# Performance work log

Measured on AMD Instinct MI355X. Metric: run time of the kernel, lower is better.

## Reference

```python
import jax, jax.numpy as jnp
import numpy as np
import math

B, T, D, H, FF, L, CS, LC = 8, 512, 512, 8, 2048, 6, 16, 4
DK = D // H
MIN16 = float(np.finfo(np.float16).min)  # masked_fill value used by the module


def _chunk_mask(size, ck, n_left):
    # subsequent_chunk_mask: row i attends [max((i//ck - n_left)*ck, 0), (i//ck + 1)*ck)
    i = np.arange(size)
    j = np.arange(size)
    ci = i // ck
    start = np.maximum((ci - n_left) * ck, 0)
    end = (ci + 1) * ck
    return (j[None, :] >= start[:, None]) & (j[None, :] < end[:, None])


def setup_inputs() -> dict:
    key = jax.random.key(0)
    ks = jax.random.split(key, 16)
    s = 0.02
    rn = lambda k, shp: jax.random.normal(k, shp, jnp.float32) * s
    xs = jax.random.normal(ks[0], (B, T, D), jnp.float32)
    # RelPositionalEncoding sinusoidal table
    pos = np.arange(T, dtype=np.float32)[:, None]
    div = np.exp(np.arange(0, D, 2, dtype=np.float32) * (-math.log(10000.0) / D))
    pe = np.zeros((T, D), np.float32)
    pe[:, 0::2] = np.sin(pos * div)
    pe[:, 1::2] = np.cos(pos * div)
    pos_emb = jnp.asarray(pe)[None]  # (1, T, D)
    mask = jnp.asarray(_chunk_mask(T, CS, LC))[None]  # (1, T, T) bool, True=attend
    return {
        'xs': xs, 'pos_emb': pos_emb, 'mask': mask,
        'Wq': rn(ks[1], (L, D, D)), 'bq': jnp.zeros((L, D)),
        'Wk': rn(ks[2], (L, D, D)), 'bk': jnp.zeros((L, D)),
        'Wv': rn(ks[3], (L, D, D)), 'bv': jnp.zeros((L, D)),
        'Wo': rn(ks[4], (L, D, D)), 'bo': jnp.zeros((L, D)),
        'Wp': rn(ks[5], (L, D, D)),
        'pbu': rn(ks[6], (L, H, DK)), 'pbv': rn(ks[7], (L, H, DK)),
        'ln1_s': jnp.ones((L, D)), 'ln1_b': jnp.zeros((L, D)),
        'ln2_s': jnp.ones((L, D)), 'ln2_b': jnp.zeros((L, D)),
        'W1': rn(ks[8], (L, D, FF)), 'b1': jnp.zeros((L, FF)),
        'W2': rn(ks[9], (L, FF, D)), 'b2': jnp.zeros((L, D)),
        'lnf_s': jnp.ones((D,)), 'lnf_b': jnp.zeros((D,)),
    }


def _ln(x, g, b):
    m = jnp.mean(x, -1, keepdims=True)
    v = jnp.var(x, -1, keepdims=True)
    return (x - m) * jax.lax.rsqrt(v + 1e-5) * g + b


def reference(xs, pos_emb, mask, Wq, bq, Wk, bk, Wv, bv, Wo, bo, Wp, pbu, pbv,
              ln1_s, ln1_b, ln2_s, ln2_b, W1, b1, W2, b2, lnf_s, lnf_b):
    x = xs * math.sqrt(D)          # xscale from positional encoding
    m = mask[:, None, :, :]        # (1,1,T,T)
    scale = 1.0 / math.sqrt(DK)
    for l in range(L):
        h = _ln(x, ln1_s[l], ln1_b[l])
        q = (h @ Wq[l] + bq[l]).reshape(B, T, H, DK)                       # (B,T,H,DK)
        k = (h @ Wk[l] + bk[l]).reshape(B, T, H, DK).transpose(0, 2, 1, 3)  # (B,H,T,DK)
        v = (h @ Wv[l] + bv[l]).reshape(B, T, H, DK).transpose(0, 2, 1, 3)
        p = (pos_emb @ Wp[l]).reshape(T, H, DK).transpose(1, 0, 2)          # (H,T,DK)
        qu = (q + pbu[l]).transpose(0, 2, 1, 3)  # (B,H,T,DK)
        qv = (q + pbv[l]).transpose(0, 2, 1, 3)
        ac = jnp.einsum('bhtd,bhsd->bhts', qu, k)
        bd = jnp.einsum('bhtd,hsd->bhts', qv, p)
        scores = jnp.where(m, (ac + bd) * scale, MIN16)
        attn = jnp.where(m, jax.nn.softmax(scores, axis=-1), 0.0)
        o = jnp.einsum('bhts,bhsd->bthd', attn, v).reshape(B, T, D)
        x = x + o @ Wo[l] + bo[l]
        h2 = _ln(x, ln2_s[l], ln2_b[l])
        x = x + jax.nn.relu(h2 @ W1[l] + b1[l]) @ W2[l] + b2[l]
    return _ln(x, lnf_s, lnf_b)
```

## Files before the change

### kernel.cpp

```cpp
#include <hip/hip_runtime.h>

#define B_ 8
#define T_ 512
#define D_ 512
#define H_ 8
#define FF_ 2048
#define L_ 6
#define CS_ 16
#define LC_ 4
#define DK_ 64
#define MT_ (B_*T_)

typedef unsigned short u16;
typedef __attribute__((ext_vector_type(8))) short bf8_t;
typedef __attribute__((ext_vector_type(4))) float f4_t;

__device__ __forceinline__ float bf2f(u16 u){
  union { unsigned int i; float f; } c; c.i = ((unsigned int)u) << 16; return c.f;
}
__device__ __forceinline__ u16 f2bf(float f){
  union { float f; unsigned int i; } c; c.f = f;
  unsigned int x = c.i;
  return (u16)((x + 0x7FFFu + ((x >> 16) & 1u)) >> 16);
}

__global__ void init_kernel(const float* __restrict__ xs, const float* __restrict__ pe,
                            float* __restrict__ x, u16* __restrict__ pe_bf)
{
  int stride = gridDim.x * blockDim.x;
  int i0 = blockIdx.x * blockDim.x + threadIdx.x;
  const float s = 22.62741699796952f;
  for (int i = i0; i < B_*T_*D_; i += stride) x[i] = xs[i] * s;
  for (int i = i0; i < T_*D_;    i += stride) pe_bf[i] = f2bf(pe[i]);
}

__global__ void transpose_kernel(const float* __restrict__ in, u16* __restrict__ out,
                                 int K, int N)
{
  __shared__ float tile[32][33];
  int l = blockIdx.z;
  const float* src = in + (size_t)l * K * N;
  u16* dst = out + (size_t)l * N * K;
  int n0 = blockIdx.x * 32, k0 = blockIdx.y * 32;
  int tx = threadIdx.x, ty = threadIdx.y;
  #pragma unroll
  for (int i = 0; i < 4; ++i)
    tile[ty + i*8][tx] = src[(size_t)(k0 + ty + i*8) * N + n0 + tx];
  __syncthreads();
  #pragma unroll
  for (int i = 0; i < 4; ++i)
    dst[(size_t)(n0 + ty + i*8) * K + k0 + tx] = f2bf(tile[tx][ty + i*8]);
}

__global__ void transpose_qkv_kernel(const float* __restrict__ Wq, const float* __restrict__ Wk,
                                     const float* __restrict__ Wv, u16* __restrict__ out)
{
  __shared__ float tile[32][33];
  int l = blockIdx.z;
  int n0 = blockIdx.x * 32, k0 = blockIdx.y * 32;
  const float* W = (n0 < 512) ? Wq : (n0 < 1024 ? Wk : Wv);
  int nn0 = n0 & 511;
  const float* src = W + (size_t)l * D_ * D_;
  u16* dst = out + (size_t)l * 3 * D_ * D_;
  int tx = threadIdx.x, ty = threadIdx.y;
  #pragma unroll
  for (int i = 0; i < 4; ++i)
    tile[ty + i*8][tx] = src[(size_t)(k0 + ty + i*8) * D_ + nn0 + tx];
  __syncthreads();
  #pragma unroll
  for (int i = 0; i < 4; ++i)
    dst[(size_t)(n0 + ty + i*8) * D_ + k0 + tx] = f2bf(tile[tx][ty + i*8]);
}

__global__ void pack_bias_kernel(const float* __restrict__ bq, const float* __restrict__ bk,
                                 const float* __restrict__ bv, float* __restrict__ out)
{
  int l = blockIdx.x, t = threadIdx.x;
  out[l*1536 + t]        = bq[l*512 + t];
  out[l*1536 + 512  + t] = bk[l*512 + t];
  out[l*1536 + 1024 + t] = bv[l*512 + t];
}

template <int OUTMODE>
__global__ __launch_bounds__(256) void ln_kernel(const float* __restrict__ x,
    const float* __restrict__ g, const float* __restrict__ b, void* __restrict__ outp)
{
  int row = blockIdx.x;
  const float* xr = x + (size_t)row * D_;
  int t = threadIdx.x;
  float v0 = xr[t], v1 = xr[t + 256];
  float s = v0 + v1, s2 = v0*v0 + v1*v1;
  #pragma unroll
  for (int off = 32; off > 0; off >>= 1){ s += __shfl_down(s, off); s2 += __shfl_down(s2, off); }
  __shared__ float ps[4], ps2[4], mb[2];
  int w = t >> 6;
  if ((t & 63) == 0){ ps[w] = s; ps2[w] = s2; }
  __syncthreads();
  if (t == 0){
    float S = ps[0]+ps[1]+ps[2]+ps[3];
    float S2 = ps2[0]+ps2[1]+ps2[2]+ps2[3];
    float m = S * (1.0f / D_);
    float var = S2 * (1.0f / D_) - m*m;
    mb[0] = m; mb[1] = rsqrtf(var + 1e-5f);
  }
  __syncthreads();
  float m = mb[0], rs = mb[1];
  float o0 = (v0 - m) * rs * g[t]     + b[t];
  float o1 = (v1 - m) * rs * g[t+256] + b[t+256];
  if (OUTMODE == 1){
    float* outr = (float*)outp + (size_t)row * D_;
    outr[t] = o0; outr[t+256] = o1;
  } else {
    u16* outr = (u16*)outp + (size_t)row * D_;
    outr[t] = f2bf(o0); outr[t+256] = f2bf(o1);
  }
}

template <int TN>
__global__ __launch_bounds__(256) void mgemm_kernel(
    const u16* __restrict__ A, const u16* __restrict__ Bt,
    const float* __restrict__ bias, const float* __restrict__ resid,
    void* __restrict__ C, int M, int N, int K,
    int relu, int bf16out, size_t wstride, size_t cstride)
{
  constexpr int NT = TN / 32;
  Bt += (size_t)blockIdx.z * wstride;
  size_t coff = (size_t)blockIdx.z * cstride;

  __shared__ u16 As[128 * 32];
  __shared__ u16 Bs[TN * 32];

  int tid  = threadIdx.x;
  int wave = tid >> 6, lane = tid & 63;
  int wm = wave >> 1, wn = wave & 1;
  int fm = lane & 15, fq = lane >> 4;

  int m0 = blockIdx.y * 128, n0 = blockIdx.x * TN;

  f4_t acc[4][NT];
  #pragma unroll
  for (int i = 0; i < 4; ++i)
    #pragma unroll
    for (int j = 0; j < NT; ++j) acc[i][j] = (f4_t)0.0f;

  int srow = lane >> 2;
  int selem = (lane & 3) << 3;

  for (int k0 = 0; k0 < K; k0 += 32){
    #pragma unroll
    for (int j = 0; j < 2; ++j){
      int c = wave * 2 + j;
      const u16* gp = A + (size_t)(m0 + c*16 + srow) * K + k0 + selem;
      u16* lp = &As[c * 512];
      __builtin_amdgcn_global_load_lds((const __attribute__((address_space(1))) void*)gp,
                                       (__attribute__((address_space(3))) void*)lp, 16, 0, 0);
    }
    #pragma unroll
    for (int j = 0; j < TN/64; ++j){
      int c = wave * (TN/64) + j;
      const u16* gp = Bt + (size_t)(n0 + c*16 + srow) * K + k0 + selem;
      u16* lp = &Bs[c * 512];
      __builtin_amdgcn_global_load_lds((const __attribute__((address_space(1))) void*)gp,
                                       (__attribute__((address_space(3))) void*)lp, 16, 0, 0);
    }
    __syncthreads();

    bf8_t af[4], bf[NT];
    #pragma unroll
    for (int mi = 0; mi < 4; ++mi)
      af[mi] = *(const bf8_t*)&As[(wm*64 + mi*16 + fm) * 32 + fq*8];
    #pragma unroll
    for (int nj = 0; nj < NT; ++nj)
      bf[nj] = *(const bf8_t*)&Bs[(wn*(TN/2) + nj*16 + fm) * 32 + fq*8];
    #pragma unroll
    for (int mi = 0; mi < 4; ++mi)
      #pragma unroll
      for (int nj = 0; nj < NT; ++nj)
        acc[mi][nj] = __builtin_amdgcn_mfma_f32_16x16x32_bf16(af[mi], bf[nj], acc[mi][nj], 0, 0, 0);
    __syncthreads();
  }

  int rbase = m0 + wm*64, cbase = n0 + wn*(TN/2);
  #pragma unroll
  for (int mi = 0; mi < 4; ++mi){
    #pragma unroll
    for (int nj = 0; nj < NT; ++nj){
      int col = cbase + nj*16 + fm;
      float bia = bias ? bias[col] : 0.0f;
      #pragma unroll
      for (int r = 0; r < 4; ++r){
        int row = rbase + mi*16 + fq*4 + r;
        size_t idx = coff + (size_t)row * N + col;
        float val = acc[mi][nj][r] + bia;
        if (relu)  val = fmaxf(val, 0.0f);
        if (resid) val += resid[idx];
        if (bf16out) ((u16*)C)[idx] = f2bf(val);
        else         ((float*)C)[idx] = val;
      }
    }
  }
}

__global__ __launch_bounds__(64) void attn_kernel(
    const u16* __restrict__ qkv, const u16* __restrict__ p,
    const float* __restrict__ pbu, const float* __restrict__ pbv,
    u16* __restrict__ o)
{
  int ci = blockIdx.x, h = blockIdx.y, b = blockIdx.z;
  int t0 = ci * CS_;
  int cb = ci - LC_; if (cb < 0) cb = 0;
  int c0 = cb * CS_;
  int ncol = (ci + 1) * CS_ - c0;

  __shared__ u16 smem[15648];
  u16* qu = smem;
  u16* qv = smem + 1024;
  u16* kp = smem + 2048;
  u16* pp = smem + 2048 + 5120;
  float* vf  = (float*)(smem + 2048);
  float* psf = (float*)(smem + 12288);

  int lane = threadIdx.x;
  int fm = lane & 15, fq = lane >> 4;

  const u16* kbase = qkv + ((size_t)(b*T_ + c0)) * 1536 + 512 + h*DK_;
  const u16* pbase = p + (size_t)c0 * D_ + h*DK_;
  int srow8 = lane >> 3, scol = (lane & 7) << 3;
  #pragma unroll
  for (int c = 0; c < 10; ++c){
    const u16* gk = kbase + (size_t)(c*8 + srow8) * 1536 + scol;
    __builtin_amdgcn_global_load_lds((const __attribute__((address_space(1))) void*)gk,
        (__attribute__((address_space(3))) void*)(kp + c*512 + lane*8), 16, 0, 0);
    const u16* gp = pbase + (size_t)(c*8 + srow8) * D_ + scol;
    __builtin_amdgcn_global_load_lds((const __attribute__((address_space(1))) void*)gp,
        (__attribute__((address_space(3))) void*)(pp + c*512 + lane*8), 16, 0, 0);
  }
  const u16* qbase = qkv + ((size_t)(b*T_ + t0)) * 1536 + h*DK_;
  #pragma unroll
  for (int it = 0; it < 4; ++it){
    int i = it*256 + lane*4; int r = i >> 6; int d = i & 63;
    ushort4 w = *(const ushort4*)(qbase + (size_t)r * 1536 + d);
    float4 bu = *(const float4*)(pbu + h*DK_ + d);
    float4 bv = *(const float4*)(pbv + h*DK_ + d);
    ushort4 ou, ov;
    ou.x = f2bf(bf2f(w.x) + bu.x); ou.y = f2bf(bf2f(w.y) + bu.y);
    ou.z = f2bf(bf2f(w.z) + bu.z); ou.w = f2bf(bf2f(w.w) + bu.w);
    ov.x = f2bf(bf2f(w.x) + bv.x); ov.y = f2bf(bf2f(w.y) + bv.y);
    ov.z = f2bf(bf2f(w.z) + bv.z); ov.w = f2bf(bf2f(w.w) + bv.w);
    *(ushort4*)(qu + r*64 + d) = ou;
    *(ushort4*)(qv + r*64 + d) = ov;
  }
  __syncthreads();

  bf8_t au0 = *(const bf8_t*)(qu + fm*64 + fq*8);
  bf8_t au1 = *(const bf8_t*)(qu + fm*64 + 32 + fq*8);
  bf8_t av0 = *(const bf8_t*)(qv + fm*64 + fq*8);
  bf8_t av1 = *(const bf8_t*)(qv + fm*64 + 32 + fq*8);
  f4_t acc[5];
  #pragma unroll
  for (int nt = 0; nt < 5; ++nt) acc[nt] = (f4_t)0.0f;
  #pragma unroll
  for (int nt = 0; nt < 5; ++nt){
    const u16* kr = kp + (nt*16 + fm)*64;
    const u16* pr = pp + (nt*16 + fm)*64;
    bf8_t bk0 = *(const bf8_t*)(kr + fq*8);
    bf8_t bk1 = *(const bf8_t*)(kr + 32 + fq*8);
    bf8_t bp0 = *(const bf8_t*)(pr + fq*8);
    bf8_t bp1 = *(const bf8_t*)(pr + 32 + fq*8);
    f4_t a = acc[nt];
    a = __builtin_amdgcn_mfma_f32_16x16x32_bf16(au0, bk0, a, 0, 0, 0);
    a = __builtin_amdgcn_mfma_f32_16x16x32_bf16(au1, bk1, a, 0, 0, 0);
    a = __builtin_amdgcn_mfma_f32_16x16x32_bf16(av0, bp0, a, 0, 0, 0);
    a = __builtin_amdgcn_mfma_f32_16x16x32_bf16(av1, bp1, a, 0, 0, 0);
    acc[nt] = a;
  }

  const float scale = 0.125f;
  float mx[4], sm[4];
  float e[5][4];
  #pragma unroll
  for (int r = 0; r < 4; ++r) mx[r] = -3.0e38f;
  #pragma unroll
  for (int nt = 0; nt < 5; ++nt){
    bool valid = (nt*16 + fm) < ncol;
    #pragma unroll
    for (int r = 0; r < 4; ++r){
      float v = valid ? acc[nt][r] : -3.0e38f;
      mx[r] = fmaxf(mx[r], v);
    }
  }
  #pragma unroll
  for (int r = 0; r < 4; ++r){
    #pragma unroll
    for (int m = 1; m < 16; m <<= 1) mx[r] = fmaxf(mx[r], __shfl_xor(mx[r], m));
    sm[r] = 0.0f;
  }
  #pragma unroll
  for (int nt = 0; nt < 5; ++nt){
    bool valid = (nt*16 + fm) < ncol;
    #pragma unroll
    for (int r = 0; r < 4; ++r){
      float ev = valid ? __expf((acc[nt][r] - mx[r]) * scale) : 0.0f;
      e[nt][r] = ev; sm[r] += ev;
    }
  }
  #pragma unroll
  for (int r = 0; r < 4; ++r){
    #pragma unroll
    for (int m = 1; m < 16; m <<= 1) sm[r] += __shfl_xor(sm[r], m);
    sm[r] = 1.0f / sm[r];
  }
  #pragma unroll
  for (int nt = 0; nt < 5; ++nt)
    #pragma unroll
    for (int r = 0; r < 4; ++r)
      psf[(fq*4 + r)*105 + nt*16 + fm] = e[nt][r] * sm[r];
  __syncthreads();

  const u16* vbase = qkv + ((size_t)(b*T_ + c0)) * 1536 + 1024 + h*DK_;
  #pragma unroll
  for (int it = 0; it < 20; ++it){
    int i = it*256 + lane*4; int s = i >> 6; int d = i & 63;
    ushort4 w = *(const ushort4*)(vbase + (size_t)s * 1536 + d);
    float4 f; f.x = bf2f(w.x); f.y = bf2f(w.y); f.z = bf2f(w.z); f.w = bf2f(w.w);
    *(float4*)(vf + s*64 + d) = f;
  }
  __syncthreads();

  float oacc[16];
  #pragma unroll
  for (int ii = 0; ii < 16; ++ii) oacc[ii] = 0.0f;
  const float* psr = psf + fm*105;
  const float* vcol = vf + fq*16;
  for (int s = 0; s < 80; ++s){
    float pv = psr[s];
    const float* vr = vcol + s*64;
    float4 v0 = *(const float4*)(vr);
    float4 v1 = *(const float4*)(vr + 4);
    float4 v2 = *(const float4*)(vr + 8);
    float4 v3 = *(const float4*)(vr + 12);
    oacc[0]  += pv*v0.x; oacc[1]  += pv*v0.y; oacc[2]  += pv*v0.z; oacc[3]  += pv*v0.w;
    oacc[4]  += pv*v1.x; oacc[5]  += pv*v1.y; oacc[6]  += pv*v1.z; oacc[7]  += pv*v1.w;
    oacc[8]  += pv*v2.x; oacc[9]  += pv*v2.y; oacc[10] += pv*v2.z; oacc[11] += pv*v2.w;
    oacc[12] += pv*v3.x; oacc[13] += pv*v3.y; oacc[14] += pv*v3.z; oacc[15] += pv*v3.w;
  }
  u16* ob = o + ((size_t)(b*T_ + t0 + fm)) * D_ + h*DK_ + fq*16;
  #pragma unroll
  for (int q4 = 0; q4 < 4; ++q4){
    ushort4 w;
    w.x = f2bf(oacc[q4*4+0]); w.y = f2bf(oacc[q4*4+1]);
    w.z = f2bf(oacc[q4*4+2]); w.w = f2bf(oacc[q4*4+3]);
    *(ushort4*)(ob + q4*4) = w;
  }
}

extern "C" void kernel_launch(void* const* d_in, const int* in_sizes, int n_in,
                              void* d_out, int out_size, void* d_ws, size_t ws_size,
                              hipStream_t stream)
{
  int s0 = (n_in >= 24) ? 0 : -1;
  const float* xs   = (const float*)d_in[0];
  const float* pe   = (const float*)d_in[1];
  const float* Wq   = (const float*)d_in[3  + s0];
  const float* bq   = (const float*)d_in[4  + s0];
  const float* Wk   = (const float*)d_in[5  + s0];
  const float* bk   = (const float*)d_in[6  + s0];
  const float* Wv   = (const float*)d_in[7  + s0];
  const float* bv   = (const float*)d_in[8  + s0];
  const float* Wo   = (const float*)d_in[9  + s0];
  const float* bo   = (const float*)d_in[10 + s0];
  const float* Wp   = (const float*)d_in[11 + s0];
  const float* pbu  = (const float*)d_in[12 + s0];
  const float* pbv  = (const float*)d_in[13 + s0];
  const float* ln1s = (const float*)d_in[14 + s0];
  const float* ln1b = (const float*)d_in[15 + s0];
  const float* ln2s = (const float*)d_in[16 + s0];
  const float* ln2b = (const float*)d_in[17 + s0];
  const float* W1   = (const float*)d_in[18 + s0];
  const float* b1   = (const float*)d_in[19 + s0];
  const float* W2   = (const float*)d_in[20 + s0];
  const float* b2   = (const float*)d_in[21 + s0];
  const float* lnfs = (const float*)d_in[22 + s0];
  const float* lnfb = (const float*)d_in[23 + s0];

  float* ws = (float*)d_ws;
  size_t cur = 0;
  float* x      = ws + cur;            cur += (size_t)MT_*D_;
  u16*   region = (u16*)(ws + cur);    cur += (size_t)MT_*FF_/2;
  u16*   qkv_bf = region;
  u16*   ff_bf  = region;
  u16*   h_bf   = (u16*)(ws + cur);    cur += (size_t)MT_*D_/2;
  u16*   ob_bf  = (u16*)(ws + cur);    cur += (size_t)MT_*D_/2;
  u16*   pe_bf  = (u16*)(ws + cur);    cur += (size_t)T_*D_/2;
  u16*   pbuf   = (u16*)(ws + cur);    cur += (size_t)L_*T_*D_/2;
  u16*   qkvt   = (u16*)(ws + cur);    cur += (size_t)L_*3*D_*D_/2;
  u16*   wot    = (u16*)(ws + cur);    cur += (size_t)L_*D_*D_/2;
  u16*   w1t    = (u16*)(ws + cur);    cur += (size_t)L_*D_*FF_/2;
  u16*   w2t    = (u16*)(ws + cur);    cur += (size_t)L_*FF_*D_/2;
  u16*   wpt    = (u16*)(ws + cur);    cur += (size_t)L_*D_*D_/2;
  float* bqkv   = ws + cur;            cur += (size_t)L_*3*D_;

  dim3 tb(32, 8);
  transpose_qkv_kernel<<<dim3(48, 16, L_), tb, 0, stream>>>(Wq, Wk, Wv, qkvt);
  transpose_kernel<<<dim3(16, 16, L_), tb, 0, stream>>>(Wo, wot, D_, D_);
  transpose_kernel<<<dim3(64, 16, L_), tb, 0, stream>>>(W1, w1t, D_, FF_);
  transpose_kernel<<<dim3(16, 64, L_), tb, 0, stream>>>(W2, w2t, FF_, D_);
  transpose_kernel<<<dim3(16, 16, L_), tb, 0, stream>>>(Wp, wpt, D_, D_);
  pack_bias_kernel<<<dim3(L_), dim3(512), 0, stream>>>(bq, bk, bv, bqkv);
  init_kernel<<<dim3(512), dim3(256), 0, stream>>>(xs, pe, x, pe_bf);

  dim3 blk(256);
  mgemm_kernel<64><<<dim3(8, 4, L_), blk, 0, stream>>>(
      pe_bf, wpt, nullptr, nullptr, pbuf, T_, D_, D_, 0, 1,
      (size_t)D_*D_, (size_t)T_*D_);

  for (int l = 0; l < L_; ++l){
    ln_kernel<0><<<dim3(MT_), blk, 0, stream>>>(x, ln1s + l*D_, ln1b + l*D_, h_bf);
    mgemm_kernel<128><<<dim3(12, 32, 1), blk, 0, stream>>>(
        h_bf, qkvt + (size_t)l*3*D_*D_, bqkv + l*3*D_, nullptr, qkv_bf,
        MT_, 3*D_, D_, 0, 1, 0, 0);
    attn_kernel<<<dim3(T_/CS_, H_, B_), dim3(64), 0, stream>>>(
        qkv_bf, pbuf + (size_t)l*T_*D_, pbu + l*H_*DK_, pbv + l*H_*DK_, ob_bf);
    mgemm_kernel<64><<<dim3(8, 32, 1), blk, 0, stream>>>(
        ob_bf, wot + (size_t)l*D_*D_, bo + l*D_, x, x, MT_, D_, D_, 0, 0, 0, 0);
    ln_kernel<0><<<dim3(MT_), blk, 0, stream>>>(x, ln2s + l*D_, ln2b + l*D_, h_bf);
    mgemm_kernel<128><<<dim3(16, 32, 1), blk, 0, stream>>>(
        h_bf, w1t + (size_t)l*D_*FF_, b1 + l*FF_, nullptr, ff_bf,
        MT_, FF_, D_, 1, 1, 0, 0);
    mgemm_kernel<64><<<dim3(8, 32, 1), blk, 0, stream>>>(
        ff_bf, w2t + (size_t)l*FF_*D_, b2 + l*D_, x, x, MT_, D_, FF_, 0, 0, 0, 0);
  }
  ln_kernel<1><<<dim3(MT_), blk, 0, stream>>>(x, lnfs, lnfb, d_out);
}
```

Baseline: 1.037 ms.

## Double-buffer GEMM LDS tiles with async prefetch; vectorize LayerNorm one row per wave

The MFMA GEMM now keeps two LDS buffers. It issues the global-to-LDS loads for the next K-slice before computing the current one, and uses explicit vmcnt waits and s_barrier in place of a full __syncthreads drain each iteration, so load latency overlaps with MFMA work. LayerNorm is rewritten so each wave handles one row with float4 loads, xor-shuffle reductions and vector stores, which removes the shared-memory reduction and block barriers. LDS use per GEMM block doubles and may lower occupancy. The hand-written waitcnt logic relies on a fixed per-thread load count being correct.

```diff
diff --git a/kernel.cpp b/kernel.cpp
--- a/kernel.cpp
+++ b/kernel.cpp
@@ -23,6 +23,10 @@
   unsigned int x = c.i;
   return (u16)((x + 0x7FFFu + ((x >> 16) & 1u)) >> 16);
 }
+__device__ __forceinline__ void ld_lds16(const u16* gp, u16* lp){
+  __builtin_amdgcn_global_load_lds((const __attribute__((address_space(1))) void*)gp,
+                                   (__attribute__((address_space(3))) void*)lp, 16, 0, 0);
+}
 
 __global__ void init_kernel(const float* __restrict__ xs, const float* __restrict__ pe,
                             float* __restrict__ x, u16* __restrict__ pe_bf)
@@ -85,34 +89,38 @@
 __global__ __launch_bounds__(256) void ln_kernel(const float* __restrict__ x,
     const float* __restrict__ g, const float* __restrict__ b, void* __restrict__ outp)
 {
-  int row = blockIdx.x;
+  int lane = threadIdx.x & 63;
+  int row  = (blockIdx.x << 2) + (threadIdx.x >> 6);
   const float* xr = x + (size_t)row * D_;
-  int t = threadIdx.x;
-  float v0 = xr[t], v1 = xr[t + 256];
-  float s = v0 + v1, s2 = v0*v0 + v1*v1;
-  #pragma unroll
-  for (int off = 32; off > 0; off >>= 1){ s += __shfl_down(s, off); s2 += __shfl_down(s2, off); }
-  __shared__ float ps[4], ps2[4], mb[2];
-  int w = t >> 6;
-  if ((t & 63) == 0){ ps[w] = s; ps2[w] = s2; }
-  __syncthreads();
-  if (t == 0){
-    float S = ps[0]+ps[1]+ps[2]+ps[3];
-    float S2 = ps2[0]+ps2[1]+ps2[2]+ps2[3];
-    float m = S * (1.0f / D_);
-    float var = S2 * (1.0f / D_) - m*m;
-    mb[0] = m; mb[1] = rsqrtf(var + 1e-5f);
-  }
-  __syncthreads();
-  float m = mb[0], rs = mb[1];
-  float o0 = (v0 - m) * rs * g[t]     + b[t];
-  float o1 = (v1 - m) * rs * g[t+256] + b[t+256];
+  int d = lane * 8;
+  float4 a0 = *(const float4*)(xr + d);
+  float4 a1 = *(const float4*)(xr + d + 4);
+  float s  = a0.x+a0.y+a0.z+a0.w + a1.x+a1.y+a1.z+a1.w;
+  float s2 = a0.x*a0.x+a0.y*a0.y+a0.z*a0.z+a0.w*a0.w
+           + a1.x*a1.x+a1.y*a1.y+a1.z*a1.z+a1.w*a1.w;
+  #pragma unroll
+  for (int off = 32; off > 0; off >>= 1){ s += __shfl_xor(s, off); s2 += __shfl_xor(s2, off); }
+  float m  = s * (1.0f / D_);
+  float var = s2 * (1.0f / D_) - m*m;
+  float rs = rsqrtf(var + 1e-5f);
+  float4 g0 = *(const float4*)(g + d), g1 = *(const float4*)(g + d + 4);
+  float4 b0 = *(const float4*)(b + d), b1 = *(const float4*)(b + d + 4);
+  float o[8];
+  o[0]=(a0.x-m)*rs*g0.x+b0.x; o[1]=(a0.y-m)*rs*g0.y+b0.y;
+  o[2]=(a0.z-m)*rs*g0.z+b0.z; o[3]=(a0.w-m)*rs*g0.w+b0.w;
+  o[4]=(a1.x-m)*rs*g1.x+b1.x; o[5]=(a1.y-m)*rs*g1.y+b1.y;
+  o[6]=(a1.z-m)*rs*g1.z+b1.z; o[7]=(a1.w-m)*rs*g1.w+b1.w;
   if (OUTMODE == 1){
-    float* outr = (float*)outp + (size_t)row * D_;
-    outr[t] = o0; outr[t+256] = o1;
+    float* outr = (float*)outp + (size_t)row * D_ + d;
+    *(float4*)(outr)     = make_float4(o[0],o[1],o[2],o[3]);
+    *(float4*)(outr + 4) = make_float4(o[4],o[5],o[6],o[7]);
   } else {
-    u16* outr = (u16*)outp + (size_t)row * D_;
-    outr[t] = f2bf(o0); outr[t+256] = f2bf(o1);
+    u16* outr = (u16*)outp + (size_t)row * D_ + d;
+    ushort4 w0, w1;
+    w0.x=f2bf(o[0]); w0.y=f2bf(o[1]); w0.z=f2bf(o[2]); w0.w=f2bf(o[3]);
+    w1.x=f2bf(o[4]); w1.y=f2bf(o[5]); w1.z=f2bf(o[6]); w1.w=f2bf(o[7]);
+    *(ushort4*)(outr)     = w0;
+    *(ushort4*)(outr + 4) = w1;
   }
 }
 
@@ -124,11 +132,13 @@
     int relu, int bf16out, size_t wstride, size_t cstride)
 {
   constexpr int NT = TN / 32;
+  constexpr int SB = TN / 64;
+  constexpr int S  = 2 + SB;
   Bt += (size_t)blockIdx.z * wstride;
   size_t coff = (size_t)blockIdx.z * cstride;
 
-  __shared__ u16 As[128 * 32];
-  __shared__ u16 Bs[TN * 32];
+  __shared__ u16 As[2][128 * 32];
+  __shared__ u16 Bs[2][TN * 32];
 
   int tid  = threadIdx.x;
   int wave = tid >> 6, lane = tid & 63;
@@ -146,38 +156,45 @@
   int srow = lane >> 2;
   int selem = (lane & 3) << 3;
 
-  for (int k0 = 0; k0 < K; k0 += 32){
+  auto stage = [&](int bufi, int k0){
     #pragma unroll
     for (int j = 0; j < 2; ++j){
       int c = wave * 2 + j;
-      const u16* gp = A + (size_t)(m0 + c*16 + srow) * K + k0 + selem;
-      u16* lp = &As[c * 512];
-      __builtin_amdgcn_global_load_lds((const __attribute__((address_space(1))) void*)gp,
-                                       (__attribute__((address_space(3))) void*)lp, 16, 0, 0);
-    }
-    #pragma unroll
-    for (int j = 0; j < TN/64; ++j){
-      int c = wave * (TN/64) + j;
-      const u16* gp = Bt + (size_t)(n0 + c*16 + srow) * K + k0 + selem;
-      u16* lp = &Bs[c * 512];
-      __builtin_amdgcn_global_load_lds((const __attribute__((address_space(1))) void*)gp,
-                                       (__attribute__((address_space(3))) void*)lp, 16, 0, 0);
-    }
-    __syncthreads();
-
-    bf8_t af[4], bf[NT];
+      ld_lds16(A + (size_t)(m0 + c*16 + srow) * K + k0 + selem, &As[bufi][c * 512]);
+    }
+    #pragma unroll
+    for (int j = 0; j < SB; ++j){
+      int c = wave * SB + j;
+      ld_lds16(Bt + (size_t)(n0 + c*16 + srow) * K + k0 + selem, &Bs[bufi][c * 512]);
+    }
+  };
+
+  stage(0, 0);
+  int buf = 0;
+  for (int k0 = 0; k0 < K; k0 += 32){
+    if (k0 + 32 < K){
+      stage(buf ^ 1, k0 + 32);
+      asm volatile("s_waitcnt vmcnt(%0)" :: "n"(S) : "memory");
+    } else {
+      asm volatile("s_waitcnt vmcnt(0)" ::: "memory");
+    }
+    asm volatile("s_barrier" ::: "memory");
+
+    bf8_t af[4], bfr[NT];
     #pragma unroll
     for (int mi = 0; mi < 4; ++mi)
-      af[mi] = *(const bf8_t*)&As[(wm*64 + mi*16 + fm) * 32 + fq*8];
+      af[mi] = *(const bf8_t*)&As[buf][(wm*64 + mi*16 + fm) * 32 + fq*8];
     #pragma unroll
     for (int nj = 0; nj < NT; ++nj)
-      bf[nj] = *(const bf8_t*)&Bs[(wn*(TN/2) + nj*16 + fm) * 32 + fq*8];
+      bfr[nj] = *(const bf8_t*)&Bs[buf][(wn*(TN/2) + nj*16 + fm) * 32 + fq*8];
     #pragma unroll
     for (int mi = 0; mi < 4; ++mi)
       #pragma unroll
       for (int nj = 0; nj < NT; ++nj)
-        acc[mi][nj] = __builtin_amdgcn_mfma_f32_16x16x32_bf16(af[mi], bf[nj], acc[mi][nj], 0, 0, 0);
-    __syncthreads();
+        acc[mi][nj] = __builtin_amdgcn_mfma_f32_16x16x32_bf16(af[mi], bfr[nj], acc[mi][nj], 0, 0, 0);
+
+    asm volatile("s_barrier" ::: "memory");
+    buf ^= 1;
   }
 
   int rbase = m0 + wm*64, cbase = n0 + wn*(TN/2);
@@ -228,12 +245,8 @@
   int srow8 = lane >> 3, scol = (lane & 7) << 3;
   #pragma unroll
   for (int c = 0; c < 10; ++c){
-    const u16* gk = kbase + (size_t)(c*8 + srow8) * 1536 + scol;
-    __builtin_amdgcn_global_load_lds((const __attribute__((address_space(1))) void*)gk,
-        (__attribute__((address_space(3))) void*)(kp + c*512 + lane*8), 16, 0, 0);
-    const u16* gp = pbase + (size_t)(c*8 + srow8) * D_ + scol;
-    __builtin_amdgcn_global_load_lds((const __attribute__((address_space(1))) void*)gp,
-        (__attribute__((address_space(3))) void*)(pp + c*512 + lane*8), 16, 0, 0);
+    ld_lds16(kbase + (size_t)(c*8 + srow8) * 1536 + scol, kp + c*512);
+    ld_lds16(pbase + (size_t)(c*8 + srow8) * D_   + scol, pp + c*512);
   }
   const u16* qbase = qkv + ((size_t)(b*T_ + t0)) * 1536 + h*DK_;
   #pragma unroll
@@ -415,7 +428,7 @@
       (size_t)D_*D_, (size_t)T_*D_);
 
   for (int l = 0; l < L_; ++l){
-    ln_kernel<0><<<dim3(MT_), blk, 0, stream>>>(x, ln1s + l*D_, ln1b + l*D_, h_bf);
+    ln_kernel<0><<<dim3(MT_/4), blk, 0, stream>>>(x, ln1s + l*D_, ln1b + l*D_, h_bf);
     mgemm_kernel<128><<<dim3(12, 32, 1), blk, 0, stream>>>(
         h_bf, qkvt + (size_t)l*3*D_*D_, bqkv + l*3*D_, nullptr, qkv_bf,
         MT_, 3*D_, D_, 0, 1, 0, 0);
@@ -423,12 +436,12 @@
         qkv_bf, pbuf + (size_t)l*T_*D_, pbu + l*H_*DK_, pbv + l*H_*DK_, ob_bf);
     mgemm_kernel<64><<<dim3(8, 32, 1), blk, 0, stream>>>(
         ob_bf, wot + (size_t)l*D_*D_, bo + l*D_, x, x, MT_, D_, D_, 0, 0, 0, 0);
-    ln_kernel<0><<<dim3(MT_), blk, 0, stream>>>(x, ln2s + l*D_, ln2b + l*D_, h_bf);
+    ln_kernel<0><<<dim3(MT_/4), blk, 0, stream>>>(x, ln2s + l*D_, ln2b + l*D_, h_bf);
     mgemm_kernel<128><<<dim3(16, 32, 1), blk, 0, stream>>>(
         h_bf, w1t + (size_t)l*D_*FF_, b1 + l*FF_, nullptr, ff_bf,
         MT_, FF_, D_, 1, 1, 0, 0);
     mgemm_kernel<64><<<dim3(8, 32, 1), blk, 0, stream>>>(
         ff_bf, w2t + (size_t)l*FF_*D_, b2 + l*D_, x, x, MT_, D_, FF_, 0, 0, 0, 0);
   }
-  ln_kernel<1><<<dim3(MT_), blk, 0, stream>>>(x, lnfs, lnfb, d_out);
-}
+  ln_kernel<1><<<dim3(MT_/4), blk, 0, stream>>>(x, lnfs, lnfb, d_out);
+}
```

Result: faster. 978.6 us (-5.6%).
